# Performance work log

Measured on AMD Instinct MI355X. Metric: run time of the kernel, lower is better.

The kernel has to match this reference:

```python
import jax, jax.numpy as jnp
import numpy as np

NG = 6      # K*2 graphs
N = 6000    # nodes per graph
E = 96000   # edges per graph
F_IN = 128  # input node feature dim
C = 128     # ggnn_args['out_channels']
BINS = 21


def setup_inputs() -> dict:
    key = jax.random.key(0)
    ks = jax.random.split(key, 5)
    x = jax.random.normal(ks[0], (NG, N, F_IN), jnp.float32)
    edge_index = jax.random.randint(ks[1], (NG, 2, E), 0, N, dtype=jnp.int64)
    edge_attr = jax.random.uniform(ks[2], (NG, E, 6), dtype=jnp.float32)
    # 4 GCNConv layers: Linear (no bias inside lin) + separate bias param
    gcn_W = jax.random.normal(ks[3], (4, F_IN, C), jnp.float32) / np.sqrt(F_IN)
    gcn_b = jnp.zeros((4, C), jnp.float32)
    # 4 xavier-init Ws matrices
    Ws = jax.random.normal(ks[4], (4, C, C), jnp.float32) / np.sqrt(C)
    return {"x": x, "edge_index": edge_index, "edge_attr": edge_attr,
            "gcn_W": gcn_W, "gcn_b": gcn_b, "Ws": Ws}


def _gcn(x, row, col, w, W, b):
    """PyG GCNConv with edge weights: add self-loops (weight 1), symmetric norm."""
    n = x.shape[0]
    loop = jnp.arange(n)
    r = jnp.concatenate([row, loop])
    c = jnp.concatenate([col, loop])
    ww = jnp.concatenate([w, jnp.ones((n,), w.dtype)])
    deg = jax.ops.segment_sum(ww, c, num_segments=n)
    dis = jnp.where(deg > 0, jax.lax.rsqrt(jnp.maximum(deg, 1e-30)), 0.0)
    norm = dis[r] * ww * dis[c]
    h = x @ W  # [n, C]
    out = jax.ops.segment_sum(norm[:, None] * h[r], c, num_segments=n)
    return out + b


def _gnn_layer(x, ei, ea, gcn_W, gcn_b, Ws):
    row, col = ei[0], ei[1]
    acc = jnp.zeros((x.shape[0], C), x.dtype)
    for i in range(4):  # fixed small structural loop
        h = jax.nn.relu(_gcn(x, row, col, ea[:, i + 2], gcn_W[i], gcn_b[i]))
        acc = acc + h @ Ws[i]
    return acc


def reference(x, edge_index, edge_attr, gcn_W, gcn_b, Ws):
    # per-graph GNN features [NG, N, C]
    feats = jax.vmap(lambda xi, ei, ea: _gnn_layer(xi, ei, ea, gcn_W, gcn_b, Ws))(
        x, edge_index, edge_attr)
    # g_matrix: concat of per-graph mean embeddings -> [1, NG*C]
    g_matrix = feats.mean(axis=1).reshape(1, NG * C)
    # L2-normalize rows (F.normalize, eps=1e-12)
    nrm = jnp.linalg.norm(feats, axis=-1, keepdims=True)
    xn = feats / jnp.maximum(nrm, 1e-12)
    centers = jnp.linspace(-1.0, 1.0, BINS, dtype=jnp.float32)  # -1.0 .. 1.0 step 0.1
    width = 2.0 / BINS  # histc bin width over [-1, 1]
    rows = []
    for i1 in range(NG):
        vals = []
        for i2 in range(NG):
            t = jnp.tanh(xn[i1] @ xn[i2].T)  # [N, N]
            idx = jnp.clip(jnp.floor((t + 1.0) / width), 0, BINS - 1).astype(jnp.int32)
            hist = jnp.bincount(idx.ravel(), length=BINS).astype(jnp.float32)
            hist = hist / (N * N)
            vals.append(jnp.dot(hist, centers))
        rows.append(jnp.stack(vals))
    sim_matrix = jnp.stack(rows)[None]  # [1, NG, NG]
    return g_matrix, sim_matrix
```

## Files before the change

kernel.cpp:

```cpp
#include <hip/hip_runtime.h>

#define NG 6
#define NN 6000
#define NE 96000
#define NPAD 6016
#define NT 47

typedef unsigned int uint;
typedef unsigned short ushort;
typedef __attribute__((ext_vector_type(8))) short short8;
typedef __attribute__((ext_vector_type(4))) float f32x4;
typedef __attribute__((ext_vector_type(2))) float f32x2;

__device__ __forceinline__ ushort f2bf(float f){
  uint u = __float_as_uint(f);
  u = (u + 0x7fffu + ((u >> 16) & 1u)) >> 16;
  return (ushort)u;
}
__device__ __forceinline__ float bf2f(uint u){ return __uint_as_float(u << 16); }

__device__ __forceinline__ void async16(const void* g, void* l){
  __builtin_amdgcn_global_load_lds(
      (const __attribute__((address_space(1))) unsigned int*)g,
      (__attribute__((address_space(3))) unsigned int*)l, 16, 0, 0);
}

__device__ __constant__ int c_i1[21] = {0,0,0,0,0,0,1,1,1,1,1,2,2,2,2,3,3,3,4,4,5};
__device__ __constant__ int c_i2[21] = {0,1,2,3,4,5,1,2,3,4,5,2,3,4,5,3,4,5,4,5,5};

__device__ __forceinline__ void stage128s(const ushort* __restrict__ gsrc, int stride,
                                          ushort* lds, int w, int lane){
  #pragma unroll
  for (int i = 0; i < 8; i++){
    int off = (w*8 + i) * 512;
    int rowi = (w*8 + i)*4 + (lane >> 4);
    int chunk = (lane & 15) ^ (rowi & 15);
    async16(gsrc + (size_t)rowi*stride + chunk*8, (void*)&lds[off]);
  }
}

__device__ __forceinline__ void stage64s(const ushort* __restrict__ gsrc,
                                         ushort* lds, int w, int lane){
  #pragma unroll
  for (int i = 0; i < 4; i++){
    int off = (w*4 + i) * 512;
    int rowi = (w*4 + i)*4 + (lane >> 4);
    int chunk = (lane & 15) ^ (rowi & 15);
    async16(gsrc + (size_t)rowi*128 + chunk*8, (void*)&lds[off]);
  }
}

__device__ __forceinline__ void mfma128(const ushort* As, const ushort* Bs,
                                        int w, int lane, f32x4 acc[4][4]){
  int q = lane >> 4, cl = lane & 15;
  int wm = w >> 1, wn = w & 1;
  #pragma unroll
  for (int ks = 0; ks < 4; ks++){
    short8 af[4], bfr[4];
    int ch = ((ks*4 + q) ^ cl) * 8;
    #pragma unroll
    for (int m = 0; m < 4; m++) af[m]  = *(const short8*)&As[(wm*64 + m*16 + cl)*128 + ch];
    #pragma unroll
    for (int n = 0; n < 4; n++) bfr[n] = *(const short8*)&Bs[(wn*64 + n*16 + cl)*128 + ch];
    #pragma unroll
    for (int m = 0; m < 4; m++)
      #pragma unroll
      for (int n = 0; n < 4; n++)
        acc[m][n] = __builtin_amdgcn_mfma_f32_16x16x32_bf16(af[m], bfr[n], acc[m][n], 0, 0, 0);
  }
}
__device__ __forceinline__ void zacc(f32x4 acc[4][4]){
  #pragma unroll
  for (int m = 0; m < 4; m++)
    #pragma unroll
    for (int n = 0; n < 4; n++) acc[m][n] = (f32x4){0.f,0.f,0.f,0.f};
}

#define TC1 10.499108f
#define TC3 (-3.4888668f)
#define TC5 1.3464888f
#define TC7 (-0.4433517f)
#define TC9 0.0833385f
__device__ __forceinline__ f32x2 psumT(const f32x4 acc[4][4]){
  f32x2 t2 = {0.f, 0.f};
  #pragma unroll
  for (int m = 0; m < 4; m++)
    #pragma unroll
    for (int n = 0; n < 4; n++)
      #pragma unroll
      for (int rp = 0; rp < 2; rp++){
        f32x2 d = { acc[m][n][rp*2], acc[m][n][rp*2+1] };
        f32x2 t = d*d;
        f32x2 qq = t*TC9 + TC7;
        qq = qq*t + TC5;
        qq = qq*t + TC3;
        qq = qq*t + TC1;
        t2 = d*qq + t2;
      }
  return t2;
}

__device__ __forceinline__ f32x2 psumT24(const f32x4 acc[2][4]){
  f32x2 t2 = {0.f, 0.f};
  #pragma unroll
  for (int m = 0; m < 2; m++)
    #pragma unroll
    for (int n = 0; n < 4; n++)
      #pragma unroll
      for (int rp = 0; rp < 2; rp++){
        f32x2 d = { acc[m][n][rp*2], acc[m][n][rp*2+1] };
        f32x2 t = d*d;
        f32x2 qq = t*TC9 + TC7;
        qq = qq*t + TC5;
        qq = qq*t + TC3;
        qq = qq*t + TC1;
        t2 = d*qq + t2;
      }
  return t2;
}

__global__ void k_zero4(float4* p, int n16){
  int i = blockIdx.x*256 + threadIdx.x;
  if (i < n16) p[i] = make_float4(0.f,0.f,0.f,0.f);
}
__global__ void k_zero1(float* p, int n){
  int i = blockIdx.x*256 + threadIdx.x;
  if (i < n) p[i] = 0.f;
}
__global__ void k_cvtx(const float4* x, uint2* xbf, int n4){
  int i = blockIdx.x*256 + threadIdx.x;
  if (i >= n4) return;
  float4 v = x[i];
  xbf[i] = make_uint2((uint)f2bf(v.x) | ((uint)f2bf(v.y) << 16),
                      (uint)f2bf(v.z) | ((uint)f2bf(v.w) << 16));
}
__global__ void k_cvt_w(const float* W, const float* Wsm, ushort* Wtc, ushort* Wstc){
  int i = blockIdx.x*256 + threadIdx.x;
  int l = i >> 14, rem = i & 16383;
  int a = rem >> 7, b = rem & 127;
  Wtc[(l << 14) + b*128 + a] = f2bf(W[i]);
  Wstc[b*512 + l*128 + a]    = f2bf(Wsm[i]);
}
__global__ void k_count(const int* ei, int* counts){
  int i = blockIdx.x*256 + threadIdx.x;
  if (i >= NG*NE) return;
  int g = i / NE, e = i - g*NE;
  atomicAdd(&counts[g*NN + ei[g*2*NE + NE + e]], 1);
}
__global__ void k_scan(const int* counts, int* offs, int* cursor){
  __shared__ int sm[256];
  int g = blockIdx.x, t = threadIdx.x;
  const int* c = counts + g*NN;
  int i0 = t*24, i1 = i0 + 24; if (i1 > NN) i1 = NN; if (i0 > NN) i0 = NN;
  int s = 0;
  for (int i = i0; i < i1; i++) s += c[i];
  sm[t] = s;
  __syncthreads();
  for (int off = 1; off < 256; off <<= 1){
    int v = (t >= off) ? sm[t - off] : 0;
    __syncthreads();
    sm[t] += v;
    __syncthreads();
  }
  int run = sm[t] - s;
  for (int i = i0; i < i1; i++){
    offs[g*NN + i] = run; cursor[g*NN + i] = run; run += c[i];
  }
}
__global__ void k_place(const int* ei, int* cursor, int2* elist2){
  int i = blockIdx.x*256 + threadIdx.x;
  if (i >= NG*NE) return;
  int g = i / NE, e = i - g*NE;
  int col = ei[g*2*NE + NE + e];
  int row = ei[g*2*NE + e];
  int pos = atomicAdd(&cursor[g*NN + col], 1);
  elist2[g*NE + pos] = make_int2(e, row);
}
__global__ void k_deg(const float* __restrict__ ea, const int* __restrict__ offs,
                      const int* __restrict__ counts, const int2* __restrict__ elist2,
                      float4* __restrict__ dis4){
  int i = blockIdx.x*256 + threadIdx.x;
  if (i >= NG*NN) return;
  int g = i / NN;
  int beg = offs[i], cnt = counts[i];
  const int2* el = elist2 + (size_t)g*NE;
  const float* eag = ea + (size_t)g*NE*6;
  float4 s = make_float4(1.f,1.f,1.f,1.f);
  for (int j = 0; j < cnt; j++){
    int e = el[beg + j].x;
    float2 wa = *(const float2*)(eag + (size_t)e*6 + 2);
    float2 wb = *(const float2*)(eag + (size_t)e*6 + 4);
    s.x += wa.x; s.y += wa.y; s.z += wb.x; s.w += wb.y;
  }
  dis4[i] = make_float4(rsqrtf(fmaxf(s.x,1e-30f)), rsqrtf(fmaxf(s.y,1e-30f)),
                        rsqrtf(fmaxf(s.z,1e-30f)), rsqrtf(fmaxf(s.w,1e-30f)));
}

__global__ __launch_bounds__(256) void k_gather1(const float* __restrict__ ea,
    const float4* __restrict__ dis4, const int* __restrict__ offs,
    const int* __restrict__ counts, const int2* __restrict__ elist2,
    const ushort* __restrict__ xbf, ushort* __restrict__ agg, int c){
  __shared__ int    sr[4][64];
  __shared__ float4 sc[4][64];
  int lane = threadIdx.x, wy = threadIdx.y;
  int nidx = blockIdx.x*4 + wy;
  int lg = nidx / NN, n = nidx - lg*NN;
  int g = c*2 + lg;
  float4 dn4 = dis4[g*NN + n];
  const uint* xrow = (const uint*)xbf + (size_t)lg*NN*64;
  uint xv = xrow[(size_t)n*64 + lane];
  f32x2 xs = {bf2f(xv & 0xffffu), bf2f(xv >> 16)};
  f32x2 a0 = xs*dn4.x, a1 = xs*dn4.y, a2 = xs*dn4.z, a3 = xs*dn4.w;
  int beg = offs[g*NN + n], cnt = counts[g*NN + n];
  const int2*  el  = elist2 + (size_t)g*NE;
  const float* eag = ea + (size_t)g*NE*6;
  for (int j0 = 0; j0 < cnt; j0 += 64){
    int take = cnt - j0; if (take > 64) take = 64;
    if (lane < take){
      int2 er = el[beg + j0 + lane];
      float2 wa = *(const float2*)(eag + (size_t)er.x*6 + 2);
      float2 wb = *(const float2*)(eag + (size_t)er.x*6 + 4);
      float4 dr = dis4[g*NN + er.y];
      sr[wy][lane] = er.y;
      sc[wy][lane] = make_float4(wa.x*dr.x, wa.y*dr.y, wb.x*dr.z, wb.y*dr.w);
    }
    int j = 0;
    for (; j + 4 <= take; j += 4){
      int r0 = sr[wy][j], r1 = sr[wy][j+1], r2 = sr[wy][j+2], r3 = sr[wy][j+3];
      float4 c0 = sc[wy][j], c1 = sc[wy][j+1], c2 = sc[wy][j+2], c3 = sc[wy][j+3];
      uint x0 = xrow[(size_t)r0*64 + lane];
      uint x1 = xrow[(size_t)r1*64 + lane];
      uint x2 = xrow[(size_t)r2*64 + lane];
      uint x3 = xrow[(size_t)r3*64 + lane];
      f32x2 v;
      v = (f32x2){bf2f(x0 & 0xffffu), bf2f(x0 >> 16)};
      a0 = v*c0.x + a0; a1 = v*c0.y + a1; a2 = v*c0.z + a2; a3 = v*c0.w + a3;
      v = (f32x2){bf2f(x1 & 0xffffu), bf2f(x1 >> 16)};
      a0 = v*c1.x + a0; a1 = v*c1.y + a1; a2 = v*c1.z + a2; a3 = v*c1.w + a3;
      v = (f32x2){bf2f(x2 & 0xffffu), bf2f(x2 >> 16)};
      a0 = v*c2.x + a0; a1 = v*c2.y + a1; a2 = v*c2.z + a2; a3 = v*c2.w + a3;
      v = (f32x2){bf2f(x3 & 0xffffu), bf2f(x3 >> 16)};
      a0 = v*c3.x + a0; a1 = v*c3.y + a1; a2 = v*c3.z + a2; a3 = v*c3.w + a3;
    }
    for (; j < take; j++){
      int r0 = sr[wy][j];
      float4 c0 = sc[wy][j];
      uint x0 = xrow[(size_t)r0*64 + lane];
      f32x2 v = (f32x2){bf2f(x0 & 0xffffu), bf2f(x0 >> 16)};
      a0 = v*c0.x + a0; a1 = v*c0.y + a1; a2 = v*c0.z + a2; a3 = v*c0.w + a3;
    }
  }
  a0 = a0*dn4.x; a1 = a1*dn4.y; a2 = a2*dn4.z; a3 = a3*dn4.w;
  uint* ag = (uint*)agg;
  ag[((size_t)((lg*4+0)*NN + n))*64 + lane] = (uint)f2bf(a0.x) | ((uint)f2bf(a0.y) << 16);
  ag[((size_t)((lg*4+1)*NN + n))*64 + lane] = (uint)f2bf(a1.x) | ((uint)f2bf(a1.y) << 16);
  ag[((size_t)((lg*4+2)*NN + n))*64 + lane] = (uint)f2bf(a2.x) | ((uint)f2bf(a2.y) << 16);
  ag[((size_t)((lg*4+3)*NN + n))*64 + lane] = (uint)f2bf(a3.x) | ((uint)f2bf(a3.y) << 16);
}

__global__ __launch_bounds__(256) void k_gemm1b(const ushort* __restrict__ agg,
    const ushort* __restrict__ Wtc, const float* __restrict__ gb,
    ushort* __restrict__ H){
  __shared__ ushort As[16384];
  __shared__ ushort Bsh[16384];
  int by = blockIdx.y;
  int lg = by >> 2, l = by & 3;
  int tid = threadIdx.x, w = tid >> 6, lane = tid & 63;
  stage128s(agg + (size_t)by*NN*128 + (size_t)blockIdx.x*16384, 128, As, w, lane);
  stage128s(Wtc + (l << 14), 128, Bsh, w, lane);
  __syncthreads();
  f32x4 acc[4][4];
  zacc(acc);
  mfma128(As, Bsh, w, lane, acc);
  int q = lane >> 4, cl = lane & 15, wm = w >> 1, wn = w & 1;
  int rowb = blockIdx.x*128 + wm*64 + q*4;
  int colb = wn*64 + cl;
  #pragma unroll
  for (int m = 0; m < 4; m++)
    #pragma unroll
    for (int n = 0; n < 4; n++)
      #pragma unroll
      for (int r = 0; r < 4; r++){
        int row = rowb + m*16 + r, col = colb + n*16;
        if (row < NN){
          float v = fmaxf(acc[m][n][r] + gb[l*128 + col], 0.f);
          H[((size_t)(lg*NN + row))*512 + l*128 + col] = f2bf(v);
        }
      }
}

__global__ __launch_bounds__(256) void k_gemm2(const ushort* __restrict__ A,
    const ushort* __restrict__ B, float* __restrict__ feats, int coff){
  __shared__ ushort As[16384];
  __shared__ ushort Bsh[16384];
  int tid = threadIdx.x, w = tid >> 6, lane = tid & 63;
  f32x4 acc[4][4];
  zacc(acc);
  #pragma unroll
  for (int kc = 0; kc < 4; kc++){
    if (kc) __syncthreads();
    stage128s(A + (size_t)blockIdx.x*128*512 + kc*128, 512, As, w, lane);
    stage128s(B + kc*128, 512, Bsh, w, lane);
    __syncthreads();
    mfma128(As, Bsh, w, lane, acc);
  }
  int q = lane >> 4, cl = lane & 15, wm = w >> 1, wn = w & 1;
  int rowb = blockIdx.x*128 + wm*64 + q*4;
  int colb = wn*64 + cl;
  #pragma unroll
  for (int m = 0; m < 4; m++)
    #pragma unroll
    for (int n = 0; n < 4; n++)
      #pragma unroll
      for (int r = 0; r < 4; r++){
        int row = rowb + m*16 + r;
        if (row < 2*NN)
          feats[(size_t)(coff + row)*128 + colb + n*16] = acc[m][n][r];
      }
}

__global__ void k_mean(const float* feats, float* out){
  int g = blockIdx.x / 48, ch = blockIdx.x - g*48;
  int c = threadIdx.x;
  float s = 0.f;
  int n0 = ch*125;
  for (int n = n0; n < n0 + 125; n++) s += feats[((size_t)(g*NN + n))*128 + c];
  atomicAdd(&out[g*128 + c], s * (1.0f/6000.0f));
}

__global__ void k_xn(const float* feats, ushort* xn){
  int lane = threadIdx.x;
  int rall = blockIdx.x*4 + threadIdx.y;
  int g = rall / NPAD, rl = rall - g*NPAD;
  uint* dst = (uint*)&xn[((size_t)(g*NPAD + rl))*128];
  if (rl < NN){
    const float2* src = (const float2*)&feats[((size_t)(g*NN + rl))*128];
    float2 v = src[lane];
    float ss = v.x*v.x + v.y*v.y;
    #pragma unroll
    for (int s = 32; s > 0; s >>= 1) ss += __shfl_xor(ss, s);
    float inv = 1.0f / fmaxf(sqrtf(ss), 1e-12f);
    dst[lane] = (uint)f2bf(v.x*inv) | ((uint)f2bf(v.y*inv) << 16);
  } else {
    dst[lane] = 0u;
  }
}

__global__ __launch_bounds__(256, 4) void k_pair(const ushort* __restrict__ xn,
                                                 float* Spart){
  __shared__ ushort Bs[2][8192];
  int bx = blockIdx.x;
  int p = bx / 94, rem = bx - p*94;
  int tr = rem >> 1, h = rem & 1;
  int i1 = c_i1[p], i2 = c_i2[p];
  bool diag = (i1 == i2);
  int start0 = diag ? 2*tr : 0;
  int cnt = 94 - start0;
  int half = cnt >> 1;
  int c0 = start0 + (h ? half : 0);
  int niter = half;
  if (niter <= 0) return;
  int tid = threadIdx.x, w = tid >> 6, lane = tid & 63;
  int q = lane >> 4, cl = lane & 15;
  const ushort* Arow = xn + ((size_t)(i1*NPAD) + tr*128 + w*32 + cl)*128;
  short8 afr[2][4];
  #pragma unroll
  for (int m = 0; m < 2; m++)
    #pragma unroll
    for (int ks = 0; ks < 4; ks++)
      afr[m][ks] = *(const short8*)&Arow[m*16*128 + ks*32 + q*8];
  const ushort* Bbase = xn + ((size_t)i2*NPAD)*128;
  stage64s(Bbase + (size_t)c0*8192, Bs[0], w, lane);
  f32x2 totw = {0.f, 0.f};
  for (int it = 0; it < niter; it++){
    int cur = it & 1;
    __syncthreads();
    if (it + 1 < niter)
      stage64s(Bbase + (size_t)(c0+it+1)*8192, Bs[1-cur], w, lane);
    f32x4 acc[2][4];
    #pragma unroll
    for (int m = 0; m < 2; m++)
      #pragma unroll
      for (int n = 0; n < 4; n++) acc[m][n] = (f32x4){0.f,0.f,0.f,0.f};
    __builtin_amdgcn_s_setprio(1);
    #pragma unroll
    for (int ks = 0; ks < 4; ks++){
      short8 bfr[4];
      int ch = ((ks*4 + q) ^ cl) * 8;
      #pragma unroll
      for (int n = 0; n < 4; n++)
        bfr[n] = *(const short8*)&Bs[cur][(n*16 + cl)*128 + ch];
      #pragma unroll
      for (int m = 0; m < 2; m++)
        #pragma unroll
        for (int n = 0; n < 4; n++)
          acc[m][n] = __builtin_amdgcn_mfma_f32_16x16x32_bf16(afr[m][ks], bfr[n], acc[m][n], 0, 0, 0);
    }
    __builtin_amdgcn_s_setprio(0);
    f32x2 t2 = psumT24(acc);
    float wgt = (diag && (c0+it) >= 2*tr + 2) ? 2.f : 1.f;
    totw = t2*wgt + totw;
  }
  float tot = totw.x + totw.y;
  #pragma unroll
  for (int s = 32; s > 0; s >>= 1) tot += __shfl_xor(tot, s);
  if (lane == 0) atomicAdd(&Spart[p*64 + (bx & 63)], tot);
}

__global__ void k_final(const float* Spart, float* out){
  int t = threadIdx.x;
  if (t < 21){
    float s = 0.f;
    for (int j = 0; j < 64; j++) s += Spart[t*64 + j];
    float v = s * (1.0f/360000000.0f);
    int i1 = c_i1[t], i2 = c_i2[t];
    out[768 + i1*6 + i2] = v;
    out[768 + i2*6 + i1] = v;
  }
}

extern "C" void kernel_launch(void* const* d_in, const int* in_sizes, int n_in,
                              void* d_out, int out_size, void* d_ws, size_t ws_size,
                              hipStream_t stream){
  (void)in_sizes; (void)n_in; (void)out_size; (void)ws_size;
  const float* x   = (const float*)d_in[0];
  const int*   ei  = (const int*)d_in[1];
  const float* ea  = (const float*)d_in[2];
  const float* gW  = (const float*)d_in[3];
  const float* gb  = (const float*)d_in[4];
  const float* Wsm = (const float*)d_in[5];
  float* out = (float*)d_out;
  char* ws = (char*)d_ws;
  float*  feats  = (float*) (ws + 0);
  int*    counts = (int*)   (ws + 18432000);
  int*    offs   = (int*)   (ws + 18576000);
  int*    cursor = (int*)   (ws + 18720000);
  float*  Spart  = (float*) (ws + 18864000);
  float4* dis4   = (float4*)(ws + 18872192);
  int2*   elist2 = (int2*)  (ws + 19448192);
  ushort* Wtc    = (ushort*)(ws + 24056192);
  ushort* Wstc   = (ushort*)(ws + 24187264);
  ushort* xbf    = (ushort*)(ws + 24318336);
  ushort* agg    = (ushort*)(ws + 27394560);
  ushort* H      = (ushort*)(ws + 39690752);
  ushort* xnbf   = (ushort*)(ws + 24318336);

  k_zero4<<<dim3(108), dim3(256), 0, stream>>>((float4*)(ws + 18432000), 27512);
  k_zero1<<<dim3(4),   dim3(256), 0, stream>>>(out, 804);
  k_cvt_w<<<dim3(256), dim3(256), 0, stream>>>(gW, Wsm, Wtc, Wstc);
  k_count<<<dim3(2250), dim3(256), 0, stream>>>(ei, counts);
  k_scan <<<dim3(6),    dim3(256), 0, stream>>>(counts, offs, cursor);
  k_place<<<dim3(2250), dim3(256), 0, stream>>>(ei, cursor, elist2);
  k_deg  <<<dim3(141),  dim3(256), 0, stream>>>(ea, offs, counts, elist2, dis4);
  for (int c = 0; c < 3; c++){
    k_cvtx   <<<dim3(1500), dim3(256), 0, stream>>>(
        (const float4*)(x + (size_t)c*2*NN*128), (uint2*)xbf, 384000);
    k_gather1<<<dim3(3000), dim3(64,4), 0, stream>>>(ea, dis4, offs, counts, elist2,
                                                     xbf, agg, c);
    k_gemm1b <<<dim3(47,8), dim3(256), 0, stream>>>(agg, Wtc, gb, H);
    k_gemm2  <<<dim3(94),   dim3(256), 0, stream>>>(H, Wstc, feats, c*2*NN);
  }
  k_mean <<<dim3(288),  dim3(128),  0, stream>>>(feats, out);
  k_xn   <<<dim3(9024), dim3(64,4), 0, stream>>>(feats, xnbf);
  k_pair <<<dim3(1974), dim3(256),  0, stream>>>(xnbf, Spart);
  k_final<<<dim3(1),    dim3(64),   0, stream>>>(Spart, out);
}
```

Baseline: 542.2 us.

## Switch pairwise similarity kernel to 32x32x16 MFMA with 256-row tiles

The pairwise tanh-sum kernel now uses 32x32x16 bf16 MFMA on 256-row A tiles held in registers instead of 16x16x32 on 128-row tiles. Per-node padding grows to 6144, and the grid is rebuilt as fixed 16-chunk column spans, with separate off-diagonal and triangular diagonal block mappings through lookup tables. The goal is to cut LDS B-fragment reads per MFMA and to balance work across blocks. The cost is more registers (launch bounds drop to 3 waves), extra padded rows to compute, and a linear search in the diagonal index mapping.

Measured after the change: 561.1 us. 1.03x slower.

```diff
diff --git a/kernel.cpp b/kernel.cpp
--- a/kernel.cpp
+++ b/kernel.cpp
@@ -3,14 +3,14 @@
 #define NG 6
 #define NN 6000
 #define NE 96000
-#define NPAD 6016
-#define NT 47
+#define NP2 6144
 
 typedef unsigned int uint;
 typedef unsigned short ushort;
 typedef __attribute__((ext_vector_type(8))) short short8;
 typedef __attribute__((ext_vector_type(4))) float f32x4;
 typedef __attribute__((ext_vector_type(2))) float f32x2;
+typedef __attribute__((ext_vector_type(16))) float f32x16;
 
 __device__ __forceinline__ ushort f2bf(float f){
   uint u = __float_as_uint(f);
@@ -27,6 +27,10 @@
 
 __device__ __constant__ int c_i1[21] = {0,0,0,0,0,0,1,1,1,1,1,2,2,2,2,3,3,3,4,4,5};
 __device__ __constant__ int c_i2[21] = {0,1,2,3,4,5,1,2,3,4,5,2,3,4,5,3,4,5,4,5,5};
+__device__ __constant__ int c_nd[15] = {1,2,3,4,5,7,8,9,10,12,13,14,16,17,19};
+__device__ __constant__ int c_dg[6]  = {0,6,11,15,18,20};
+__device__ __constant__ int c_dcum[25] = {0,6,12,18,24,29,34,39,44,48,52,56,60,
+                                          63,66,69,72,74,76,78,80,81,82,83,84};
 
 __device__ __forceinline__ void stage128s(const ushort* __restrict__ gsrc, int stride,
                                           ushort* lds, int w, int lane){
@@ -81,42 +85,17 @@
 #define TC5 1.3464888f
 #define TC7 (-0.4433517f)
 #define TC9 0.0833385f
-__device__ __forceinline__ f32x2 psumT(const f32x4 acc[4][4]){
-  f32x2 t2 = {0.f, 0.f};
-  #pragma unroll
-  for (int m = 0; m < 4; m++)
-    #pragma unroll
-    for (int n = 0; n < 4; n++)
-      #pragma unroll
-      for (int rp = 0; rp < 2; rp++){
-        f32x2 d = { acc[m][n][rp*2], acc[m][n][rp*2+1] };
-        f32x2 t = d*d;
-        f32x2 qq = t*TC9 + TC7;
-        qq = qq*t + TC5;
-        qq = qq*t + TC3;
-        qq = qq*t + TC1;
-        t2 = d*qq + t2;
-      }
-  return t2;
-}
-
-__device__ __forceinline__ f32x2 psumT24(const f32x4 acc[2][4]){
-  f32x2 t2 = {0.f, 0.f};
-  #pragma unroll
-  for (int m = 0; m < 2; m++)
-    #pragma unroll
-    for (int n = 0; n < 4; n++)
-      #pragma unroll
-      for (int rp = 0; rp < 2; rp++){
-        f32x2 d = { acc[m][n][rp*2], acc[m][n][rp*2+1] };
-        f32x2 t = d*d;
-        f32x2 qq = t*TC9 + TC7;
-        qq = qq*t + TC5;
-        qq = qq*t + TC3;
-        qq = qq*t + TC1;
-        t2 = d*qq + t2;
-      }
-  return t2;
+__device__ __forceinline__ void polyacc(const f32x16 a, f32x2& t2){
+  #pragma unroll
+  for (int j = 0; j < 8; j++){
+    f32x2 d = { a[2*j], a[2*j+1] };
+    f32x2 t = d*d;
+    f32x2 qq = t*TC9 + TC7;
+    qq = qq*t + TC5;
+    qq = qq*t + TC3;
+    qq = qq*t + TC1;
+    t2 = d*qq + t2;
+  }
 }
 
 __global__ void k_zero4(float4* p, int n16){
@@ -331,8 +310,8 @@
 __global__ void k_xn(const float* feats, ushort* xn){
   int lane = threadIdx.x;
   int rall = blockIdx.x*4 + threadIdx.y;
-  int g = rall / NPAD, rl = rall - g*NPAD;
-  uint* dst = (uint*)&xn[((size_t)(g*NPAD + rl))*128];
+  int g = rall / NP2, rl = rall - g*NP2;
+  uint* dst = (uint*)&xn[((size_t)(g*NP2 + rl))*128];
   if (rl < NN){
     const float2* src = (const float2*)&feats[((size_t)(g*NN + rl))*128];
     float2 v = src[lane];
@@ -346,30 +325,38 @@
   }
 }
 
-__global__ __launch_bounds__(256, 4) void k_pair(const ushort* __restrict__ xn,
+__global__ __launch_bounds__(256, 3) void k_pair(const ushort* __restrict__ xn,
                                                  float* Spart){
   __shared__ ushort Bs[2][8192];
   int bx = blockIdx.x;
-  int p = bx / 94, rem = bx - p*94;
-  int tr = rem >> 1, h = rem & 1;
+  int p, rt, c0, niter; bool diag;
+  if (bx < 2160){
+    int pp = bx / 144, rem = bx - pp*144;
+    rt = rem / 6; int ch = rem - rt*6;
+    p = c_nd[pp]; diag = false; c0 = ch*16; niter = 16;
+  } else {
+    int idd = bx - 2160;
+    int pd = idd / 84, rem = idd - pd*84;
+    int r_ = 0;
+    while (c_dcum[r_ + 1] <= rem) r_++;
+    rt = r_;
+    int ch = rem - c_dcum[rt];
+    p = c_dg[pd]; diag = true;
+    c0 = 4*rt + ch*16;
+    int left = 96 - c0;
+    niter = left < 16 ? left : 16;
+  }
   int i1 = c_i1[p], i2 = c_i2[p];
-  bool diag = (i1 == i2);
-  int start0 = diag ? 2*tr : 0;
-  int cnt = 94 - start0;
-  int half = cnt >> 1;
-  int c0 = start0 + (h ? half : 0);
-  int niter = half;
-  if (niter <= 0) return;
   int tid = threadIdx.x, w = tid >> 6, lane = tid & 63;
-  int q = lane >> 4, cl = lane & 15;
-  const ushort* Arow = xn + ((size_t)(i1*NPAD) + tr*128 + w*32 + cl)*128;
-  short8 afr[2][4];
+  int hl = lane >> 5, l5 = lane & 31;
+  const ushort* Arow = xn + ((size_t)i1*NP2 + rt*256 + w*64 + l5)*128;
+  short8 afr[2][8];
   #pragma unroll
   for (int m = 0; m < 2; m++)
     #pragma unroll
-    for (int ks = 0; ks < 4; ks++)
-      afr[m][ks] = *(const short8*)&Arow[m*16*128 + ks*32 + q*8];
-  const ushort* Bbase = xn + ((size_t)i2*NPAD)*128;
+    for (int ks = 0; ks < 8; ks++)
+      afr[m][ks] = *(const short8*)&Arow[m*32*128 + ks*16 + hl*8];
+  const ushort* Bbase = xn + ((size_t)i2*NP2)*128;
   stage64s(Bbase + (size_t)c0*8192, Bs[0], w, lane);
   f32x2 totw = {0.f, 0.f};
   for (int it = 0; it < niter; it++){
@@ -377,28 +364,34 @@
     __syncthreads();
     if (it + 1 < niter)
       stage64s(Bbase + (size_t)(c0+it+1)*8192, Bs[1-cur], w, lane);
-    f32x4 acc[2][4];
+    f32x16 acc[2][2];
     #pragma unroll
     for (int m = 0; m < 2; m++)
       #pragma unroll
-      for (int n = 0; n < 4; n++) acc[m][n] = (f32x4){0.f,0.f,0.f,0.f};
+      for (int n = 0; n < 2; n++)
+        #pragma unroll
+        for (int e = 0; e < 16; e++) acc[m][n][e] = 0.f;
     __builtin_amdgcn_s_setprio(1);
     #pragma unroll
-    for (int ks = 0; ks < 4; ks++){
-      short8 bfr[4];
-      int ch = ((ks*4 + q) ^ cl) * 8;
-      #pragma unroll
-      for (int n = 0; n < 4; n++)
-        bfr[n] = *(const short8*)&Bs[cur][(n*16 + cl)*128 + ch];
+    for (int ks = 0; ks < 8; ks++){
+      short8 bfr[2];
+      int chnk = ks*2 + hl;
+      #pragma unroll
+      for (int n = 0; n < 2; n++){
+        int r = n*32 + l5;
+        bfr[n] = *(const short8*)&Bs[cur][r*128 + ((chnk ^ (r & 15))*8)];
+      }
       #pragma unroll
       for (int m = 0; m < 2; m++)
         #pragma unroll
-        for (int n = 0; n < 4; n++)
-          acc[m][n] = __builtin_amdgcn_mfma_f32_16x16x32_bf16(afr[m][ks], bfr[n], acc[m][n], 0, 0, 0);
+        for (int n = 0; n < 2; n++)
+          acc[m][n] = __builtin_amdgcn_mfma_f32_32x32x16_bf16(afr[m][ks], bfr[n], acc[m][n], 0, 0, 0);
     }
     __builtin_amdgcn_s_setprio(0);
-    f32x2 t2 = psumT24(acc);
-    float wgt = (diag && (c0+it) >= 2*tr + 2) ? 2.f : 1.f;
+    f32x2 t2 = {0.f, 0.f};
+    polyacc(acc[0][0], t2); polyacc(acc[0][1], t2);
+    polyacc(acc[1][0], t2); polyacc(acc[1][1], t2);
+    float wgt = (diag && (c0 + it) >= 4*rt + 4) ? 2.f : 1.f;
     totw = t2*wgt + totw;
   }
   float tot = totw.x + totw.y;
@@ -461,7 +454,7 @@
     k_gemm2  <<<dim3(94),   dim3(256), 0, stream>>>(H, Wstc, feats, c*2*NN);
   }
   k_mean <<<dim3(288),  dim3(128),  0, stream>>>(feats, out);
-  k_xn   <<<dim3(9024), dim3(64,4), 0, stream>>>(feats, xnbf);
-  k_pair <<<dim3(1974), dim3(256),  0, stream>>>(xnbf, Spart);
+  k_xn   <<<dim3(9216), dim3(64,4), 0, stream>>>(feats, xnbf);
+  k_pair <<<dim3(2664), dim3(256),  0, stream>>>(xnbf, Spart);
   k_final<<<dim3(1),    dim3(64),   0, stream>>>(Spart, out);
 }
```
